# Kernel optimization log

Measured on AMD Instinct MI355X. Metric: run time of the kernel, lower is better.

## Reference

```python
import jax, jax.numpy as jnp
import numpy as np

B, T, V, E, U = 64, 128, 20000, 512, 1024


def _gru_dir(x_tbe, W, Uw, bi, bh):
    """Keras GRU (reset_after=True, gate order z,r,h). x_tbe: [T,B,E]."""
    # Precompute all input projections in one big GEMM: [T,B,3U]
    xg = jnp.einsum('tbe,eg->tbg', x_tbe, W) + bi

    def step(h, xg_t):
        hg = h @ Uw + bh                       # [B,3U]
        xz, xr, xh = jnp.split(xg_t, 3, axis=-1)
        hz, hr, hh = jnp.split(hg, 3, axis=-1)
        z = jax.nn.sigmoid(xz + hz)            # update gate
        r = jax.nn.sigmoid(xr + hr)            # reset gate
        hcand = jnp.tanh(xh + r * hh)          # reset_after=True form
        h_new = z * h + (1.0 - z) * hcand
        return h_new, h_new

    h0 = jnp.zeros((x_tbe.shape[1], Uw.shape[0]), x_tbe.dtype)
    hT, outs = jax.lax.scan(step, h0, xg)      # outs: [T,B,U]
    return outs, hT


def setup_inputs() -> dict:
    key = jax.random.key(0)
    ks = jax.random.split(key, 8)
    s_in = 1.0 / np.sqrt(E)
    s_rec = 1.0 / np.sqrt(U)
    return {
        'tokens': jax.random.randint(ks[0], (B, T), 0, V),
        'emb': jax.random.normal(ks[1], (V, E), jnp.float32) * 0.05,
        'Wf': jax.random.normal(ks[2], (E, 3 * U), jnp.float32) * s_in,
        'Uf': jax.random.normal(ks[3], (U, 3 * U), jnp.float32) * s_rec,
        'bif': jnp.zeros((3 * U,), jnp.float32),
        'bhf': jnp.zeros((3 * U,), jnp.float32),
        'Wb': jax.random.normal(ks[4], (E, 3 * U), jnp.float32) * s_in,
        'Ub': jax.random.normal(ks[5], (U, 3 * U), jnp.float32) * s_rec,
        'bib': jnp.zeros((3 * U,), jnp.float32),
        'bhb': jnp.zeros((3 * U,), jnp.float32),
    }


def reference(tokens, emb, Wf, Uf, bif, bhf, Wb, Ub, bib, bhb):
    tokens = tokens[:, ::-1]                    # tf.reverse(inputs, [-1])
    x = emb[tokens]                             # embedding lookup -> [B,T,E]
    x_t = jnp.swapaxes(x, 0, 1)                 # [T,B,E]
    out_f, h_f = _gru_dir(x_t, Wf, Uf, bif, bhf)
    out_b, h_b = _gru_dir(x_t[::-1], Wb, Ub, bib, bhb)
    out_b = out_b[::-1]                         # re-align backward outputs
    outputs = jnp.swapaxes(out_f + out_b, 0, 1)  # merge_mode='sum' -> [B,T,U]
    hidden = jnp.concatenate([h_f, h_b], axis=1)  # [B,2U]
    return outputs, hidden
```

## Files before the change

kernel.cpp:

```cpp
#include <hip/hip_runtime.h>
#include <hip/hip_bf16.h>

typedef float f32;
typedef __hip_bfloat16 bf16;
typedef unsigned int u32;
typedef unsigned short u16;

#define T_LEN 128
#define B_SZ  64
#define E_DIM 512
#define U_DIM 1024
#define G3    3072
#define BTU   (B_SZ * T_LEN * U_DIM)

typedef __attribute__((ext_vector_type(8))) __bf16 bf16x8;
typedef __attribute__((ext_vector_type(8))) u16  us8;
typedef __attribute__((ext_vector_type(4))) u16  us4;
typedef __attribute__((ext_vector_type(4))) f32  f32x4;

union F8 { us8 u; bf16x8 b; };

#define WS_USW 0u
#define WS_HQ  25165824u
#define WS_XG  26214400u


#define STEP_LDS 98304
#define XG_LDS   65536

__device__ __forceinline__ u32 f32_to_bf16_rne(f32 x) {
  u32 b = __float_as_uint(x);
  return (b + 0x7fffu + ((b >> 16) & 1u)) >> 16;
}

__global__ __launch_bounds__(256) void transpose_split(
    const f32* __restrict__ Uf, const f32* __restrict__ Ub, u16* __restrict__ USW)
{
  __shared__ f32 tile[32][33];
  const int d = blockIdx.z;
  const f32* Uw = d ? Ub : Uf;
  const int c0 = blockIdx.x * 32;
  const int k0 = blockIdx.y * 32;
  const int tx = threadIdx.x & 31;
  const int ty = threadIdx.x >> 5;
#pragma unroll
  for (int i = 0; i < 4; i++) {
    int kl = ty + i * 8;
    tile[kl][tx] = Uw[(size_t)(k0 + kl) * G3 + c0 + tx];
  }
  __syncthreads();
#pragma unroll
  for (int i = 0; i < 4; i++) {
    int cl = ty + i * 8;
    int c  = c0 + cl;
    f32 val = tile[tx][cl];
    int g = c >> 10, u = c & 1023;
    int blk = d * 128 + (u >> 3);
    int r   = g * 8 + (u & 7);
    u32 hib = f32_to_bf16_rne(val);
    f32 rem = val - __uint_as_float(hib << 16);
    u32 lob = f32_to_bf16_rne(rem);
    int k = k0 + tx;
    int slot = (k >> 3) ^ (r & 7);
    size_t base = ((size_t)blk * 2) * (24 * 1024);
    size_t off  = (size_t)r * 1024 + slot * 8 + (k & 7);
    USW[base + off] = (u16)hib;
    USW[base + (size_t)24 * 1024 + off] = (u16)lob;
  }
}

__global__ __launch_bounds__(256) void split_w(
    const f32* __restrict__ Wf, const f32* __restrict__ Wb, u16* __restrict__ WT)
{
  __shared__ f32 tile[32][33];
  const int d = blockIdx.z;
  const f32* W = d ? Wb : Wf;
  const int c0 = blockIdx.x * 32;
  const int k0 = blockIdx.y * 32;
  const int tx = threadIdx.x & 31;
  const int ty = threadIdx.x >> 5;
#pragma unroll
  for (int i = 0; i < 4; i++) {
    int kl = ty + i * 8;
    tile[kl][tx] = W[(size_t)(k0 + kl) * G3 + c0 + tx];
  }
  __syncthreads();
#pragma unroll
  for (int i = 0; i < 4; i++) {
    int cl = ty + i * 8;
    f32 val = tile[tx][cl];
    u32 bb = __float_as_uint(val);
    u16 hi = (u16)(bb >> 16);
    f32 rem = val - __uint_as_float(bb & 0xffff0000u);
    u16 lo = (u16)f32_to_bf16_rne(rem);
    size_t ch = (((size_t)(d * 2 + 0) * G3) + c0 + cl) * 512 + k0 + tx;
    size_t cl_ = (((size_t)(d * 2 + 1) * G3) + c0 + cl) * 512 + k0 + tx;
    WT[ch] = hi;
    WT[cl_] = lo;
  }
}

__global__ __launch_bounds__(128) void split_emb(
    const int* __restrict__ tokens, const f32* __restrict__ emb, u16* __restrict__ XE)
{
  const int row = blockIdx.x;
  const int b = row >> 7, t = row & 127;
  const int tok = tokens[(size_t)b * T_LEN + t];
  const int k = threadIdx.x * 4;
  float4 v = *(const float4*)(emb + (size_t)tok * E_DIM + k);
  f32 vv[4] = {v.x, v.y, v.z, v.w};
  us4 h4, l4;
#pragma unroll
  for (int e = 0; e < 4; e++) {
    u32 bb = __float_as_uint(vv[e]);
    h4[e] = (u16)(bb >> 16);
    f32 rem = vv[e] - __uint_as_float(bb & 0xffff0000u);
    l4[e] = (u16)f32_to_bf16_rne(rem);
  }
  *(us4*)(XE + ((size_t)(0 * 64 + b) * 128 + t) * 512 + k) = h4;
  *(us4*)(XE + ((size_t)(1 * 64 + b) * 128 + t) * 512 + k) = l4;
}

__global__ __launch_bounds__(256) void xg_gemm_mfma2(
    const u16* __restrict__ XE,
    const u16* __restrict__ WT,
    const f32* __restrict__ bif, const f32* __restrict__ bib,
    bf16* __restrict__ XG)
{
  extern __shared__ u16 XL[];
  u16* Ash = XL;
  u16* Bsh = XL + 16384;

  const int tid = threadIdx.x;
  const int n0 = blockIdx.x * 128;
  const int by = blockIdx.y;
  const int dir = by >> 6;
  const int s0 = (by & 63) * 2;
  const f32* bi = dir ? bib : bif;

  const int wv = tid >> 6;
  const int lane = tid & 63;
  const int arow = tid >> 1;
  const int akoff = (tid & 1) * 32;
  const int bcol = tid & 127;
  const int bkoff = (tid >> 7) * 32;

  const int srow = s0 + (arow >> 6);
  const int ab = arow & 63;
  const int at = dir ? srow : (T_LEN - 1 - srow);
  const u16* asrc_h = XE + ((size_t)(0 * 64 + ab) * 128 + at) * 512 + akoff;
  const u16* asrc_l = XE + ((size_t)(1 * 64 + ab) * 128 + at) * 512 + akoff;
  const u16* bsrc_h = WT + ((size_t)(dir * 2 + 0) * G3 + n0 + bcol) * 512 + bkoff;
  const u16* bsrc_l = WT + ((size_t)(dir * 2 + 1) * G3 + n0 + bcol) * 512 + bkoff;

  f32x4 acc[2][8];
#pragma unroll
  for (int mi = 0; mi < 2; mi++)
#pragma unroll
    for (int ni = 0; ni < 8; ni++) acc[mi][ni] = (f32x4){0.f, 0.f, 0.f, 0.f};

  for (int kk = 0; kk < 8; kk++) {
    __syncthreads();
#pragma unroll
    for (int g = 0; g < 4; g++) {
      us8 h8 = *(const us8*)(asrc_h + kk * 64 + g * 8);
      us8 l8 = *(const us8*)(asrc_l + kk * 64 + g * 8);
      int sl = (((akoff >> 3) + g) ^ (arow & 7)) * 8;
      *(us8*)&Ash[(size_t)arow * 64 + sl] = h8;
      *(us8*)&Ash[(size_t)(128 + arow) * 64 + sl] = l8;
    }
#pragma unroll
    for (int g = 0; g < 4; g++) {
      us8 h8 = *(const us8*)(bsrc_h + kk * 64 + g * 8);
      us8 l8 = *(const us8*)(bsrc_l + kk * 64 + g * 8);
      int sl = (((bkoff >> 3) + g) ^ (bcol & 7)) * 8;
      *(us8*)&Bsh[(size_t)bcol * 64 + sl] = h8;
      *(us8*)&Bsh[(size_t)(128 + bcol) * 64 + sl] = l8;
    }
    __syncthreads();
#pragma unroll
    for (int ks = 0; ks < 2; ks++) {
      F8 ah[2], al[2];
#pragma unroll
      for (int mi = 0; mi < 2; mi++) {
        int row = wv * 32 + mi * 16 + (lane & 15);
        int sl = ((ks * 4 + (lane >> 4)) ^ (row & 7)) * 8;
        ah[mi].u = *(const us8*)&Ash[(size_t)row * 64 + sl];
        al[mi].u = *(const us8*)&Ash[(size_t)(128 + row) * 64 + sl];
      }
#pragma unroll
      for (int ni = 0; ni < 8; ni++) {
        int col = ni * 16 + (lane & 15);
        int sl = ((ks * 4 + (lane >> 4)) ^ (col & 7)) * 8;
        F8 bh, bl;
        bh.u = *(const us8*)&Bsh[(size_t)col * 64 + sl];
        bl.u = *(const us8*)&Bsh[(size_t)(128 + col) * 64 + sl];
#pragma unroll
        for (int mi = 0; mi < 2; mi++) {
          acc[mi][ni] = __builtin_amdgcn_mfma_f32_16x16x32_bf16(ah[mi].b, bh.b, acc[mi][ni], 0, 0, 0);
          acc[mi][ni] = __builtin_amdgcn_mfma_f32_16x16x32_bf16(ah[mi].b, bl.b, acc[mi][ni], 0, 0, 0);
          acc[mi][ni] = __builtin_amdgcn_mfma_f32_16x16x32_bf16(al[mi].b, bh.b, acc[mi][ni], 0, 0, 0);
        }
      }
    }
  }
#pragma unroll
  for (int ni = 0; ni < 8; ni++) {
    int ncol = n0 + ni * 16 + (lane & 15);
    f32 bv = bi[ncol];
#pragma unroll
    for (int mi = 0; mi < 2; mi++) {
#pragma unroll
      for (int j = 0; j < 4; j++) {
        int row = wv * 32 + mi * 16 + (lane >> 4) * 4 + j;
        int sr = s0 + (row >> 6);
        int b = row & 63;
        XG[((size_t)(dir * T_LEN + sr) * B_SZ + b) * G3 + ncol] =
            __float2bfloat16(acc[mi][ni][j] + bv);
      }
    }
  }
}

__global__ __launch_bounds__(512) void gru_step6(
    const u16* __restrict__ USW,
    u16* __restrict__ Hq2,
    const u16* __restrict__ XG,
    const f32* __restrict__ bhf, const f32* __restrict__ bhb,
    f32* __restrict__ out, int s)
{
  extern __shared__ u16 Us[];
  const int blk = blockIdx.x;
  const int dir = blk >> 7;
  const int su  = (blk & 127) * 8;
  const int tid = threadIdx.x;
  const int lane = tid & 63;
  const int w  = tid >> 6;
  const int nw = w & 3, kw = w >> 2;

  {
    const us8* src = (const us8*)(USW + (size_t)blk * (2 * 24 * 1024));
    us8* dst = (us8*)Us;
    for (int i = tid; i < 6144; i += 512) dst[i] = src[i];
  }

  const int bb = nw * 16 + (lane & 15);
  const int ko = (lane >> 4) * 8;
  const int kq = kw * 512;
  const int r0 = lane & 15;
  const int r1t = 16 + (lane & 15);
  const int r1 = r1t > 23 ? 23 : r1t;

  const int rb_h0 = (0 * 24 + r0) * 2048;
  const int rb_l0 = (1 * 24 + r0) * 2048;
  const int rb_h1 = (0 * 24 + r1) * 2048;
  const int rb_l1 = (1 * 24 + r1) * 2048;
  const int sw0 = r0 & 7, sw1 = r1 & 7;

  const int bufr = s & 1, bufw = bufr ^ 1;
  const u16* HrHi = Hq2 + (size_t)(((bufr * 2 + 0) * 2 + dir) * 64 + bb) * 1024;
  const u16* HrLo = Hq2 + (size_t)(((bufr * 2 + 1) * 2 + dir) * 64 + bb) * 1024;

  __syncthreads();

  f32x4 acc0 = {0.f, 0.f, 0.f, 0.f};
  f32x4 acc1 = {0.f, 0.f, 0.f, 0.f};

  if (s) {
    for (int ks = 0; ks < 16; ks++) {
      const int kb = kq + ks * 32;
      const int slot = (kb >> 3) + (lane >> 4);
      F8 ah0, al0, ah1, al1;
      ah0.u = *(const us8*)((const char*)Us + rb_h0 + ((slot ^ sw0) << 4));
      al0.u = *(const us8*)((const char*)Us + rb_l0 + ((slot ^ sw0) << 4));
      ah1.u = *(const us8*)((const char*)Us + rb_h1 + ((slot ^ sw1) << 4));
      al1.u = *(const us8*)((const char*)Us + rb_l1 + ((slot ^ sw1) << 4));

      F8 bh_hi, bh_lo;
      bh_hi.u = *(const us8*)(HrHi + kb + ko);
      bh_lo.u = *(const us8*)(HrLo + kb + ko);

      acc0 = __builtin_amdgcn_mfma_f32_16x16x32_bf16(ah0.b, bh_hi.b, acc0, 0, 0, 0);
      acc0 = __builtin_amdgcn_mfma_f32_16x16x32_bf16(ah0.b, bh_lo.b, acc0, 0, 0, 0);
      acc0 = __builtin_amdgcn_mfma_f32_16x16x32_bf16(al0.b, bh_hi.b, acc0, 0, 0, 0);
      acc1 = __builtin_amdgcn_mfma_f32_16x16x32_bf16(ah1.b, bh_hi.b, acc1, 0, 0, 0);
      acc1 = __builtin_amdgcn_mfma_f32_16x16x32_bf16(ah1.b, bh_lo.b, acc1, 0, 0, 0);
      acc1 = __builtin_amdgcn_mfma_f32_16x16x32_bf16(al1.b, bh_hi.b, acc1, 0, 0, 0);
    }
  }

  __syncthreads();
  f32* red = (f32*)Us;
  if (kw == 1) {
    f32* p = red + (size_t)(nw * 64 + lane) * 8;
    *(f32x4*)p = acc0;
    *(f32x4*)(p + 4) = acc1;
  }
  __syncthreads();
  if (kw == 0) {
    const f32* p = red + (size_t)(nw * 64 + lane) * 8;
    f32x4 o0 = *(const f32x4*)p;
    f32x4 o1 = *(const f32x4*)(p + 4);
#pragma unroll
    for (int i = 0; i < 4; i++) { acc0[i] += o0[i]; acc1[i] += o1[i]; }

    f32 racc[4];
#pragma unroll
    for (int j = 0; j < 4; j++) racc[j] = __shfl_xor(acc0[j], 32);

    if (lane < 32) {
      const int ul0 = (lane >> 4) * 4;
      const int u0 = su + ul0;
      const u16* xgp = XG + ((size_t)(dir * T_LEN + s) * B_SZ + bb) * G3;
      us4 gz = *(const us4*)(xgp + u0);
      us4 gr = *(const us4*)(xgp + 1024 + u0);
      us4 gh = *(const us4*)(xgp + 2048 + u0);
      us4 ohi = {0, 0, 0, 0}, olo = {0, 0, 0, 0};
      if (s) {
        ohi = *(const us4*)(HrHi + u0);
        olo = *(const us4*)(HrLo + u0);
      }
      const f32* bh = dir ? bhb : bhf;
      f32x4 hnv;
      us4 whi, wlo;
#pragma unroll
      for (int j = 0; j < 4; j++) {
        const int u = u0 + j;
        f32 hz = acc0[j] + bh[u];
        f32 hr = racc[j] + bh[1024 + u];
        f32 hh = acc1[j] + bh[2048 + u];
        f32 xz = __uint_as_float((u32)gz[j] << 16);
        f32 xr = __uint_as_float((u32)gr[j] << 16);
        f32 xh = __uint_as_float((u32)gh[j] << 16);
        f32 hold = __uint_as_float((u32)ohi[j] << 16) + __uint_as_float((u32)olo[j] << 16);

        f32 z  = 1.f / (1.f + expf(-(xz + hz)));
        f32 r  = 1.f / (1.f + expf(-(xr + hr)));
        f32 hc = tanhf(xh + r * hh);
        f32 hnew = z * hold + (1.f - z) * hc;

        u32 hib = f32_to_bf16_rne(hnew);
        f32 rem = hnew - __uint_as_float(hib << 16);
        u32 lob = f32_to_bf16_rne(rem);
        hnv[j] = hnew;
        whi[j] = (u16)hib;
        wlo[j] = (u16)lob;
      }
      u16* HwHi = Hq2 + (size_t)(((bufw * 2 + 0) * 2 + dir) * 64 + bb) * 1024;
      u16* HwLo = Hq2 + (size_t)(((bufw * 2 + 1) * 2 + dir) * 64 + bb) * 1024;
      *(us4*)(HwHi + u0) = whi;
      *(us4*)(HwLo + u0) = wlo;

      const int t = dir ? (T_LEN - 1 - s) : s;
      f32* op = out + ((size_t)bb * T_LEN + t) * U_DIM + u0;
      if (s < 64) {
        *(f32x4*)op = hnv;
      } else {
        f32x4 prev = *(const f32x4*)op;
#pragma unroll
        for (int j = 0; j < 4; j++) prev[j] += hnv[j];
        *(f32x4*)op = prev;
      }
      if (s == T_LEN - 1)
        *(f32x4*)(out + (size_t)BTU + (size_t)bb * 2048 + dir * 1024 + u0) = hnv;
    }
  }
}

extern "C" void kernel_launch(void* const* d_in, const int* in_sizes, int n_in,
                              void* d_out, int out_size, void* d_ws, size_t ws_size,
                              hipStream_t stream) {
  (void)in_sizes; (void)n_in; (void)out_size; (void)ws_size;
  const int* tokens = (const int*)d_in[0];
  const f32* emb = (const f32*)d_in[1];
  const f32* Wf  = (const f32*)d_in[2];
  const f32* Uf  = (const f32*)d_in[3];
  const f32* bif = (const f32*)d_in[4];
  const f32* bhf = (const f32*)d_in[5];
  const f32* Wb  = (const f32*)d_in[6];
  const f32* Ub  = (const f32*)d_in[7];
  const f32* bib = (const f32*)d_in[8];
  const f32* bhb = (const f32*)d_in[9];

  char* ws = (char*)d_ws;
  u16*  USW = (u16*)(ws + WS_USW);
  u16*  Hq2 = (u16*)(ws + WS_HQ);
  bf16* XG  = (bf16*)(ws + WS_XG);
  f32*  out = (f32*)d_out;

  u16* WT = (u16*)d_out;
  u16* XE = (u16*)((char*)d_out + 12582912);

  split_w<<<dim3(96, 16, 2), 256, 0, stream>>>(Wf, Wb, WT);
  split_emb<<<8192, 128, 0, stream>>>(tokens, emb, XE);
  transpose_split<<<dim3(96, 32, 2), 256, 0, stream>>>(Uf, Ub, USW);

  hipFuncSetAttribute((const void*)xg_gemm_mfma2,
                      hipFuncAttributeMaxDynamicSharedMemorySize, XG_LDS);
  xg_gemm_mfma2<<<dim3(24, 128), 256, XG_LDS, stream>>>(XE, WT, bif, bib, XG);

  hipFuncSetAttribute((const void*)gru_step6,
                      hipFuncAttributeMaxDynamicSharedMemorySize, STEP_LDS);
  for (int s = 0; s < T_LEN; s++)
    gru_step6<<<256, 512, STEP_LDS, stream>>>(USW, Hq2, (const u16*)XG, bhf, bhb, out, s);
}
```

Baseline: 2.275 ms.

## Replace per-timestep GRU launches with persistent cooperative kernel and grid barrier

The recurrence previously ran as 128 separate kernel launches, and each launch reloaded its recurrent-weight slice into LDS. It now runs as one cooperative persistent kernel that loads the weights once and loops over timesteps. Steps are separated by a two-level atomic grid barrier: 32 strided counters, plus a release flag that block 0 sets. The hidden state layout also changes to packed hi/lo bf16 in u32, transposed to [k][batch]. As a result the MFMA operand loads become 8 strided scalar gathers instead of one vector load. This removes launch and weight-reload overhead, at the cost of spin-wait barrier latency and less coalesced hidden-state reads.

New measurement: 3.019 ms. 1.33x slower.

```diff
diff --git a/kernel.cpp b/kernel.cpp
--- a/kernel.cpp
+++ b/kernel.cpp
@@ -23,9 +23,10 @@
 #define WS_USW 0u
 #define WS_HQ  25165824u
 #define WS_XG  26214400u
-
-
-#define STEP_LDS 98304
+#define WS_BAR 126877696u
+
+
+#define PERS_LDS 106496
 #define XG_LDS   65536
 
 __device__ __forceinline__ u32 f32_to_bf16_rne(f32 x) {
@@ -222,12 +223,13 @@
   }
 }
 
-__global__ __launch_bounds__(512) void gru_step6(
+__global__ __launch_bounds__(512) void gru_persist2(
     const u16* __restrict__ USW,
-    u16* __restrict__ Hq2,
+    u32* __restrict__ Hq,
     const u16* __restrict__ XG,
     const f32* __restrict__ bhf, const f32* __restrict__ bhb,
-    f32* __restrict__ out, int s)
+    f32* __restrict__ out,
+    u32* __restrict__ bar)
 {
   extern __shared__ u16 Us[];
   const int blk = blockIdx.x;
@@ -246,7 +248,6 @@
 
   const int bb = nw * 16 + (lane & 15);
   const int ko = (lane >> 4) * 8;
-  const int kq = kw * 512;
   const int r0 = lane & 15;
   const int r1t = 16 + (lane & 15);
   const int r1 = r1t > 23 ? 23 : r1t;
@@ -257,113 +258,138 @@
   const int rb_l1 = (1 * 24 + r1) * 2048;
   const int sw0 = r0 & 7, sw1 = r1 & 7;
 
-  const int bufr = s & 1, bufw = bufr ^ 1;
-  const u16* HrHi = Hq2 + (size_t)(((bufr * 2 + 0) * 2 + dir) * 64 + bb) * 1024;
-  const u16* HrLo = Hq2 + (size_t)(((bufr * 2 + 1) * 2 + dir) * 64 + bb) * 1024;
+  f32* red = (f32*)(Us + 49152);
+  const f32* bh = dir ? bhb : bhf;
 
   __syncthreads();
 
-  f32x4 acc0 = {0.f, 0.f, 0.f, 0.f};
-  f32x4 acc1 = {0.f, 0.f, 0.f, 0.f};
-
-  if (s) {
-    for (int ks = 0; ks < 16; ks++) {
-      const int kb = kq + ks * 32;
-      const int slot = (kb >> 3) + (lane >> 4);
-      F8 ah0, al0, ah1, al1;
-      ah0.u = *(const us8*)((const char*)Us + rb_h0 + ((slot ^ sw0) << 4));
-      al0.u = *(const us8*)((const char*)Us + rb_l0 + ((slot ^ sw0) << 4));
-      ah1.u = *(const us8*)((const char*)Us + rb_h1 + ((slot ^ sw1) << 4));
-      al1.u = *(const us8*)((const char*)Us + rb_l1 + ((slot ^ sw1) << 4));
-
-      F8 bh_hi, bh_lo;
-      bh_hi.u = *(const us8*)(HrHi + kb + ko);
-      bh_lo.u = *(const us8*)(HrLo + kb + ko);
-
-      acc0 = __builtin_amdgcn_mfma_f32_16x16x32_bf16(ah0.b, bh_hi.b, acc0, 0, 0, 0);
-      acc0 = __builtin_amdgcn_mfma_f32_16x16x32_bf16(ah0.b, bh_lo.b, acc0, 0, 0, 0);
-      acc0 = __builtin_amdgcn_mfma_f32_16x16x32_bf16(al0.b, bh_hi.b, acc0, 0, 0, 0);
-      acc1 = __builtin_amdgcn_mfma_f32_16x16x32_bf16(ah1.b, bh_hi.b, acc1, 0, 0, 0);
-      acc1 = __builtin_amdgcn_mfma_f32_16x16x32_bf16(ah1.b, bh_lo.b, acc1, 0, 0, 0);
-      acc1 = __builtin_amdgcn_mfma_f32_16x16x32_bf16(al1.b, bh_hi.b, acc1, 0, 0, 0);
-    }
-  }
-
-  __syncthreads();
-  f32* red = (f32*)Us;
-  if (kw == 1) {
-    f32* p = red + (size_t)(nw * 64 + lane) * 8;
-    *(f32x4*)p = acc0;
-    *(f32x4*)(p + 4) = acc1;
-  }
-  __syncthreads();
-  if (kw == 0) {
-    const f32* p = red + (size_t)(nw * 64 + lane) * 8;
-    f32x4 o0 = *(const f32x4*)p;
-    f32x4 o1 = *(const f32x4*)(p + 4);
-#pragma unroll
-    for (int i = 0; i < 4; i++) { acc0[i] += o0[i]; acc1[i] += o1[i]; }
-
-    f32 racc[4];
-#pragma unroll
-    for (int j = 0; j < 4; j++) racc[j] = __shfl_xor(acc0[j], 32);
-
-    if (lane < 32) {
-      const int ul0 = (lane >> 4) * 4;
-      const int u0 = su + ul0;
-      const u16* xgp = XG + ((size_t)(dir * T_LEN + s) * B_SZ + bb) * G3;
-      us4 gz = *(const us4*)(xgp + u0);
-      us4 gr = *(const us4*)(xgp + 1024 + u0);
-      us4 gh = *(const us4*)(xgp + 2048 + u0);
-      us4 ohi = {0, 0, 0, 0}, olo = {0, 0, 0, 0};
-      if (s) {
-        ohi = *(const us4*)(HrHi + u0);
-        olo = *(const us4*)(HrLo + u0);
-      }
-      const f32* bh = dir ? bhb : bhf;
-      f32x4 hnv;
-      us4 whi, wlo;
-#pragma unroll
-      for (int j = 0; j < 4; j++) {
-        const int u = u0 + j;
-        f32 hz = acc0[j] + bh[u];
-        f32 hr = racc[j] + bh[1024 + u];
-        f32 hh = acc1[j] + bh[2048 + u];
-        f32 xz = __uint_as_float((u32)gz[j] << 16);
-        f32 xr = __uint_as_float((u32)gr[j] << 16);
-        f32 xh = __uint_as_float((u32)gh[j] << 16);
-        f32 hold = __uint_as_float((u32)ohi[j] << 16) + __uint_as_float((u32)olo[j] << 16);
-
-        f32 z  = 1.f / (1.f + expf(-(xz + hz)));
-        f32 r  = 1.f / (1.f + expf(-(xr + hr)));
-        f32 hc = tanhf(xh + r * hh);
-        f32 hnew = z * hold + (1.f - z) * hc;
-
-        u32 hib = f32_to_bf16_rne(hnew);
-        f32 rem = hnew - __uint_as_float(hib << 16);
-        u32 lob = f32_to_bf16_rne(rem);
-        hnv[j] = hnew;
-        whi[j] = (u16)hib;
-        wlo[j] = (u16)lob;
-      }
-      u16* HwHi = Hq2 + (size_t)(((bufw * 2 + 0) * 2 + dir) * 64 + bb) * 1024;
-      u16* HwLo = Hq2 + (size_t)(((bufw * 2 + 1) * 2 + dir) * 64 + bb) * 1024;
-      *(us4*)(HwHi + u0) = whi;
-      *(us4*)(HwLo + u0) = wlo;
-
-      const int t = dir ? (T_LEN - 1 - s) : s;
-      f32* op = out + ((size_t)bb * T_LEN + t) * U_DIM + u0;
-      if (s < 64) {
-        *(f32x4*)op = hnv;
-      } else {
-        f32x4 prev = *(const f32x4*)op;
-#pragma unroll
-        for (int j = 0; j < 4; j++) prev[j] += hnv[j];
-        *(f32x4*)op = prev;
-      }
-      if (s == T_LEN - 1)
-        *(f32x4*)(out + (size_t)BTU + (size_t)bb * 2048 + dir * 1024 + u0) = hnv;
-    }
+  for (int s = 0; s < T_LEN; s++) {
+    const u32* Hin  = Hq + (size_t)((s & 1) * 2 + dir) * (U_DIM * B_SZ);
+    u32*       Hout = Hq + (size_t)(((s + 1) & 1) * 2 + dir) * (U_DIM * B_SZ);
+
+    f32x4 acc0 = {0.f, 0.f, 0.f, 0.f};
+    f32x4 acc1 = {0.f, 0.f, 0.f, 0.f};
+
+    if (s) {
+      for (int ks = 0; ks < 16; ks++) {
+        const int kb = kw * 512 + ks * 32;
+        const int slot = (kb >> 3) + (lane >> 4);
+        F8 ah0, al0, ah1, al1;
+        ah0.u = *(const us8*)((const char*)Us + rb_h0 + ((slot ^ sw0) << 4));
+        al0.u = *(const us8*)((const char*)Us + rb_l0 + ((slot ^ sw0) << 4));
+        ah1.u = *(const us8*)((const char*)Us + rb_h1 + ((slot ^ sw1) << 4));
+        al1.u = *(const us8*)((const char*)Us + rb_l1 + ((slot ^ sw1) << 4));
+
+        const int kbase = kb + ko;
+        u32 wd[8];
+#pragma unroll
+        for (int e = 0; e < 8; e++) wd[e] = Hin[(size_t)(kbase + e) * B_SZ + bb];
+        F8 bh_hi, bh_lo;
+#pragma unroll
+        for (int e = 0; e < 8; e++) {
+          bh_hi.u[e] = (u16)(wd[e] & 0xffffu);
+          bh_lo.u[e] = (u16)(wd[e] >> 16);
+        }
+        acc0 = __builtin_amdgcn_mfma_f32_16x16x32_bf16(ah0.b, bh_hi.b, acc0, 0, 0, 0);
+        acc0 = __builtin_amdgcn_mfma_f32_16x16x32_bf16(ah0.b, bh_lo.b, acc0, 0, 0, 0);
+        acc0 = __builtin_amdgcn_mfma_f32_16x16x32_bf16(al0.b, bh_hi.b, acc0, 0, 0, 0);
+        acc1 = __builtin_amdgcn_mfma_f32_16x16x32_bf16(ah1.b, bh_hi.b, acc1, 0, 0, 0);
+        acc1 = __builtin_amdgcn_mfma_f32_16x16x32_bf16(ah1.b, bh_lo.b, acc1, 0, 0, 0);
+        acc1 = __builtin_amdgcn_mfma_f32_16x16x32_bf16(al1.b, bh_hi.b, acc1, 0, 0, 0);
+      }
+    }
+
+    __syncthreads();
+    if (kw == 1) {
+      f32* p = red + (size_t)(nw * 64 + lane) * 8;
+      *(f32x4*)p = acc0;
+      *(f32x4*)(p + 4) = acc1;
+    }
+    __syncthreads();
+    if (kw == 0) {
+      const f32* p = red + (size_t)(nw * 64 + lane) * 8;
+      f32x4 o0 = *(const f32x4*)p;
+      f32x4 o1 = *(const f32x4*)(p + 4);
+#pragma unroll
+      for (int i = 0; i < 4; i++) { acc0[i] += o0[i]; acc1[i] += o1[i]; }
+
+      f32 racc[4];
+#pragma unroll
+      for (int j = 0; j < 4; j++) racc[j] = __shfl_xor(acc0[j], 32);
+
+      if (lane < 32) {
+        const int ul0 = (lane >> 4) * 4;
+        const int u0 = su + ul0;
+        const u16* xgp = XG + ((size_t)(dir * T_LEN + s) * B_SZ + bb) * G3;
+        us4 gz = *(const us4*)(xgp + u0);
+        us4 gr = *(const us4*)(xgp + 1024 + u0);
+        us4 gh = *(const us4*)(xgp + 2048 + u0);
+        f32x4 hnv;
+#pragma unroll
+        for (int j = 0; j < 4; j++) {
+          const int u = u0 + j;
+          f32 hz = acc0[j] + bh[u];
+          f32 hr = racc[j] + bh[1024 + u];
+          f32 hh = acc1[j] + bh[2048 + u];
+          f32 xz = __uint_as_float((u32)gz[j] << 16);
+          f32 xr = __uint_as_float((u32)gr[j] << 16);
+          f32 xh = __uint_as_float((u32)gh[j] << 16);
+
+          u32 hw = s ? Hin[(size_t)u * B_SZ + bb] : 0u;
+          f32 hold = __uint_as_float(hw << 16) + __uint_as_float(hw & 0xffff0000u);
+
+          f32 z  = 1.f / (1.f + expf(-(xz + hz)));
+          f32 r  = 1.f / (1.f + expf(-(xr + hr)));
+          f32 hc = tanhf(xh + r * hh);
+          f32 hnew = z * hold + (1.f - z) * hc;
+
+          u32 hib = f32_to_bf16_rne(hnew);
+          f32 rem = hnew - __uint_as_float(hib << 16);
+          u32 lob = f32_to_bf16_rne(rem);
+          Hout[(size_t)u * B_SZ + bb] = hib | (lob << 16);
+          hnv[j] = hnew;
+        }
+
+        const int t = dir ? (T_LEN - 1 - s) : s;
+        f32* op = out + ((size_t)bb * T_LEN + t) * U_DIM + u0;
+        if (s < 64) {
+          *(f32x4*)op = hnv;
+        } else {
+          f32x4 prev = *(const f32x4*)op;
+#pragma unroll
+          for (int j = 0; j < 4; j++) prev[j] += hnv[j];
+          *(f32x4*)op = prev;
+        }
+        if (s == T_LEN - 1)
+          *(f32x4*)(out + (size_t)BTU + (size_t)bb * 2048 + dir * 1024 + u0) = hnv;
+      }
+    }
+
+    __syncthreads();
+    if (tid == 0) {
+      __threadfence();
+      __hip_atomic_fetch_add(&bar[(blk & 31) * 32], 1u,
+                             __ATOMIC_RELAXED, __HIP_MEMORY_SCOPE_AGENT);
+    }
+    if (blk == 0) {
+      if (tid < 32) {
+        const u32 tgt = (u32)(s + 1) * 8u;
+        while (__hip_atomic_load(&bar[tid * 32], __ATOMIC_RELAXED,
+                                 __HIP_MEMORY_SCOPE_AGENT) < tgt)
+          __builtin_amdgcn_s_sleep(1);
+      }
+      __syncthreads();
+      if (tid == 0)
+        __hip_atomic_store(&bar[1024], (u32)(s + 1),
+                           __ATOMIC_RELAXED, __HIP_MEMORY_SCOPE_AGENT);
+    }
+    if (tid == 0) {
+      while (__hip_atomic_load(&bar[1024], __ATOMIC_RELAXED,
+                               __HIP_MEMORY_SCOPE_AGENT) < (u32)(s + 1))
+        __builtin_amdgcn_s_sleep(1);
+      __threadfence();
+    }
+    __syncthreads();
   }
 }
 
@@ -384,13 +410,15 @@
 
   char* ws = (char*)d_ws;
   u16*  USW = (u16*)(ws + WS_USW);
-  u16*  Hq2 = (u16*)(ws + WS_HQ);
+  u32*  Hq  = (u32*)(ws + WS_HQ);
   bf16* XG  = (bf16*)(ws + WS_XG);
+  u32*  bar = (u32*)(ws + WS_BAR);
   f32*  out = (f32*)d_out;
 
   u16* WT = (u16*)d_out;
   u16* XE = (u16*)((char*)d_out + 12582912);
 
+  hipMemsetAsync(bar, 0, 8192, stream);
   split_w<<<dim3(96, 16, 2), 256, 0, stream>>>(Wf, Wb, WT);
   split_emb<<<8192, 128, 0, stream>>>(tokens, emb, XE);
   transpose_split<<<dim3(96, 32, 2), 256, 0, stream>>>(Uf, Ub, USW);
@@ -399,8 +427,17 @@
                       hipFuncAttributeMaxDynamicSharedMemorySize, XG_LDS);
   xg_gemm_mfma2<<<dim3(24, 128), 256, XG_LDS, stream>>>(XE, WT, bif, bib, XG);
 
-  hipFuncSetAttribute((const void*)gru_step6,
-                      hipFuncAttributeMaxDynamicSharedMemorySize, STEP_LDS);
-  for (int s = 0; s < T_LEN; s++)
-    gru_step6<<<256, 512, STEP_LDS, stream>>>(USW, Hq2, (const u16*)XG, bhf, bhb, out, s);
-}
+  hipFuncSetAttribute((const void*)gru_persist2,
+                      hipFuncAttributeMaxDynamicSharedMemorySize, PERS_LDS);
+  const u16* usw_a = USW;
+  u32*       hq_a  = Hq;
+  const u16* xg_a  = (const u16*)XG;
+  const f32* bhf_a = bhf;
+  const f32* bhb_a = bhb;
+  f32*       out_a = out;
+  u32*       bar_a = bar;
+  void* kargs[] = { (void*)&usw_a, (void*)&hq_a, (void*)&xg_a,
+                    (void*)&bhf_a, (void*)&bhb_a, (void*)&out_a, (void*)&bar_a };
+  hipLaunchCooperativeKernel((const void*)gru_persist2, dim3(256), dim3(512),
+                             kargs, PERS_LDS, stream);
+}
```
